# Kernel tuning notes

Measured on AMD Instinct MI355X. Metric: run time of the kernel, lower is better.

Reference implementation:

```python
import jax, jax.numpy as jnp
import numpy as np
from jax.ops import segment_sum

IN_DIM, HID_DIM, OUT_DIM = 128, 128, 64
N_NODES, N_EDGES = 50000, 800000


def gcn_conv(x, src, dst, W, b, n_nodes):
    # Symmetric GCN normalization (no self loops): deg at targets from unit weights
    deg = segment_sum(jnp.ones(src.shape[0], dtype=x.dtype), dst, num_segments=n_nodes)
    dinv = jnp.where(deg > 0, jax.lax.rsqrt(jnp.maximum(deg, 1.0)), 0.0)
    norm = dinv[src] * dinv[dst]                      # [E]
    h = x @ W                                         # [N, out] small GEMM first (PyG order)
    msg = h[src] * norm[:, None]                      # gather + scale: [E, out]
    out = segment_sum(msg, dst, num_segments=n_nodes) # scatter-add to targets
    return out + b


def setup_inputs() -> dict:
    key = jax.random.key(0)
    k1, k2, k3, k4, k5 = jax.random.split(key, 5)
    x = jax.random.normal(k1, (N_NODES, IN_DIM), dtype=jnp.float32)
    edge_index = jax.random.randint(k2, (2, N_EDGES), 0, N_NODES, dtype=jnp.int64)
    s1 = 1.0 / np.sqrt(IN_DIM)
    s2 = 1.0 / np.sqrt(HID_DIM)
    W1 = jax.random.uniform(k3, (IN_DIM, HID_DIM), jnp.float32, -s1, s1)
    b1 = jnp.zeros((HID_DIM,), jnp.float32)
    W2 = jax.random.uniform(k4, (HID_DIM, OUT_DIM), jnp.float32, -s2, s2)
    b2 = jnp.zeros((OUT_DIM,), jnp.float32)
    return {"x": x, "edge_index": edge_index, "W1": W1, "b1": b1, "W2": W2, "b2": b2}


def reference(x, edge_index, W1, b1, W2, b2):
    n_nodes = x.shape[0]
    src, dst = edge_index[0], edge_index[1]
    h = gcn_conv(x, src, dst, W1, b1, n_nodes)
    h = jax.nn.relu(h)
    # Dropout is identity in eval mode (reference is deterministic)
    out = gcn_conv(h, src, dst, W2, b2, n_nodes)
    return out
```

## Files before the change

kernel.cpp:

```cpp
#include <hip/hip_runtime.h>

#define N_NODES 50000
#define N_EDGES 800000
#define IN_DIM  128
#define HID_DIM 128
#define OUT_DIM 64

#define NPAD 50176
#define NB 7
#define KEYS (N_NODES * NB)
#define KPAD 350208
#define NB_SCAN2 (KPAD / 1024)
#define FILLB ((N_EDGES / 4 + 255) / 256)
#define DINVB (NPAD / 256)

typedef __attribute__((ext_vector_type(8))) short bf16x8;
typedef __attribute__((ext_vector_type(4))) float f32x4;

__device__ __forceinline__ unsigned short f2bf(float f) {
    unsigned u = __float_as_uint(f);
    u += 0x7fffu + ((u >> 16) & 1u);
    return (unsigned short)(u >> 16);
}
__device__ __forceinline__ float bflo(unsigned u) { return __uint_as_float(u << 16); }
__device__ __forceinline__ float bfhi(unsigned u) { return __uint_as_float(u & 0xffff0000u); }

#define ACC8(u)  do { \
    acc[0] += bflo(u.x); acc[1] += bfhi(u.x); \
    acc[2] += bflo(u.y); acc[3] += bfhi(u.y); \
    acc[4] += bflo(u.z); acc[5] += bfhi(u.z); \
    acc[6] += bflo(u.w); acc[7] += bfhi(u.w); } while (0)


__global__ void rank_hist_kernel(const int* __restrict__ src, const int* __restrict__ dst,
                                 int* __restrict__ cnt2, int* __restrict__ rank) {
    int e = (blockIdx.x * 256 + threadIdx.x) * 4;
    if (e >= N_EDGES) return;
    int4 s4 = *(const int4*)(src + e);
    int4 d4 = *(const int4*)(dst + e);
    int k0 = d4.x * NB + (s4.x >> 13);
    int k1 = d4.y * NB + (s4.y >> 13);
    int k2 = d4.z * NB + (s4.z >> 13);
    int k3 = d4.w * NB + (s4.w >> 13);
    int r0 = atomicAdd(&cnt2[k0], 1);
    int r1 = atomicAdd(&cnt2[k1], 1);
    int r2 = atomicAdd(&cnt2[k2], 1);
    int r3 = atomicAdd(&cnt2[k3], 1);
    *(int4*)(rank + e) = make_int4(r0, r1, r2, r3);
}


__global__ __launch_bounds__(1024) void reduce_kernel(const int* __restrict__ cnt2,
                                                      int* __restrict__ blockSums) {
    __shared__ int s[1024];
    int i = blockIdx.x * 1024 + threadIdx.x;
    s[threadIdx.x] = (i < KEYS) ? cnt2[i] : 0;
    __syncthreads();
    for (int off = 512; off > 0; off >>= 1) {
        if (threadIdx.x < off) s[threadIdx.x] += s[threadIdx.x + off];
        __syncthreads();
    }
    if (threadIdx.x == 0) blockSums[blockIdx.x] = s[0];
}

__global__ __launch_bounds__(1024) void scan_kernel(const int* __restrict__ cnt2,
                                                    const int* __restrict__ blockSums,
                                                    int* __restrict__ rs) {
    __shared__ int s[1024];
    __shared__ int sums[NB_SCAN2];
    __shared__ int base_s;
    if (threadIdx.x < NB_SCAN2) sums[threadIdx.x] = blockSums[threadIdx.x];
    int i = blockIdx.x * 1024 + threadIdx.x;
    int v = (i < KEYS) ? cnt2[i] : 0;
    s[threadIdx.x] = v;
    __syncthreads();
    if (threadIdx.x == 0) {
        int run = 0;
        for (int b = 0; b < (int)blockIdx.x; ++b) run += sums[b];
        base_s = run;
    }
    for (int off = 1; off < 1024; off <<= 1) {
        int t = (threadIdx.x >= off) ? s[threadIdx.x - off] : 0;
        __syncthreads();
        s[threadIdx.x] += t;
        __syncthreads();
    }
    if (i < KEYS) rs[i] = base_s + s[threadIdx.x] - v;
}


__global__ void fill_kernel(const int* __restrict__ src, const int* __restrict__ dst,
                            const int* __restrict__ rank, const int* __restrict__ rs,
                            int* __restrict__ csr_src, int* __restrict__ rs_mut,
                            float* __restrict__ dinv,
                            const float* __restrict__ W1, const float* __restrict__ W2,
                            unsigned short* __restrict__ w1t, unsigned short* __restrict__ w2t) {
    int bid = blockIdx.x;
    if (bid < FILLB) {
        int e = (bid * 256 + threadIdx.x) * 4;
        if (e >= N_EDGES) return;
        int4 s4 = *(const int4*)(src + e);
        int4 d4 = *(const int4*)(dst + e);
        int4 r4 = *(const int4*)(rank + e);
        csr_src[rs[d4.x * NB + (s4.x >> 13)] + r4.x] = s4.x;
        csr_src[rs[d4.y * NB + (s4.y >> 13)] + r4.y] = s4.y;
        csr_src[rs[d4.z * NB + (s4.z >> 13)] + r4.z] = s4.z;
        csr_src[rs[d4.w * NB + (s4.w >> 13)] + r4.w] = s4.w;
    } else if (bid < FILLB + 16) {
        int idx = (bid - FILLB) * 256 + threadIdx.x;
        int c = idx >> 5, k4 = (idx & 31) * 4;
        ushort4 o;
        o.x = f2bf(W1[(k4 + 0) * 128 + c]);
        o.y = f2bf(W1[(k4 + 1) * 128 + c]);
        o.z = f2bf(W1[(k4 + 2) * 128 + c]);
        o.w = f2bf(W1[(k4 + 3) * 128 + c]);
        *(ushort4*)(w1t + c * 128 + k4) = o;
    } else if (bid < FILLB + 24) {
        int idx = (bid - FILLB - 16) * 256 + threadIdx.x;
        if (idx >= 64 * 32) return;
        int c = idx >> 5, k4 = (idx & 31) * 4;
        ushort4 o;
        o.x = f2bf(W2[(k4 + 0) * 64 + c]);
        o.y = f2bf(W2[(k4 + 1) * 64 + c]);
        o.z = f2bf(W2[(k4 + 2) * 64 + c]);
        o.w = f2bf(W2[(k4 + 3) * 64 + c]);
        *(ushort4*)(w2t + c * 128 + k4) = o;
    } else {
        int d = (bid - FILLB - 24) * 256 + threadIdx.x;
        if (d == 0) rs_mut[KEYS] = N_EDGES;
        if (d < N_NODES) {
            int start = rs[d * NB];
            int end = (d == N_NODES - 1) ? N_EDGES : rs[d * NB + NB];
            int deg = end - start;
            dinv[d] = (deg > 0) ? rsqrtf((float)deg) : 0.0f;
        }
    }
}


__global__ __launch_bounds__(256) void gemm1_mfma(const float* __restrict__ x,
                                                  const unsigned short* __restrict__ w1t,
                                                  const float* __restrict__ dinv,
                                                  unsigned short* __restrict__ h1b) {
    int wave = threadIdx.x >> 6;
    int lane = threadIdx.x & 63;
    int n = lane & 15, quad = lane >> 4;
    int row0 = blockIdx.x * 64 + wave * 16;

    int arow = row0 + n;
    if (arow >= N_NODES) arow = N_NODES - 1;
    const float* aptr = x + (size_t)arow * 128 + quad * 8;
    const unsigned short* bbase = w1t + (size_t)n * 128 + quad * 8;

    f32x4 acc[8];
#pragma unroll
    for (int t = 0; t < 8; ++t) acc[t] = (f32x4){0.f, 0.f, 0.f, 0.f};

#pragma unroll
    for (int w4 = 0; w4 < 4; ++w4) {
        float4 f0 = *(const float4*)(aptr + w4 * 32);
        float4 f1 = *(const float4*)(aptr + w4 * 32 + 4);
        bf16x8 af;
        af[0] = (short)f2bf(f0.x); af[1] = (short)f2bf(f0.y);
        af[2] = (short)f2bf(f0.z); af[3] = (short)f2bf(f0.w);
        af[4] = (short)f2bf(f1.x); af[5] = (short)f2bf(f1.y);
        af[6] = (short)f2bf(f1.z); af[7] = (short)f2bf(f1.w);
#pragma unroll
        for (int t = 0; t < 8; ++t) {
            bf16x8 bf = *(const bf16x8*)(bbase + (size_t)t * 2048 + w4 * 32);
            acc[t] = __builtin_amdgcn_mfma_f32_16x16x32_bf16(af, bf, acc[t], 0, 0, 0);
        }
    }

#pragma unroll
    for (int r = 0; r < 4; ++r) {
        int row = row0 + quad * 4 + r;
        if (row < N_NODES) {
            float dn = dinv[row];
            unsigned short* o = h1b + (size_t)row * 128 + n;
#pragma unroll
            for (int t = 0; t < 8; ++t) o[t * 16] = f2bf(acc[t][r] * dn);
        }
    }
}


#define A1T_STRIDE 136

__global__ __launch_bounds__(256) void agg1_gemm2_fused(const int* __restrict__ csr_src,
                                                        const int* __restrict__ rs,
                                                        const float* __restrict__ dinv,
                                                        const float* __restrict__ b1,
                                                        const unsigned short* __restrict__ h1b,
                                                        const unsigned short* __restrict__ w2t,
                                                        unsigned short* __restrict__ h2b) {
    __shared__ unsigned short a1t[16 * A1T_STRIDE];

    int node0 = blockIdx.x * 16;
    int g = threadIdx.x >> 4;
    int q = threadIdx.x & 15;
    int node = node0 + g;
    int start = rs[node * NB];
    int m = rs[node * NB + NB] - start;

    float acc[8] = {};
    int j = 0;
    for (; j + 7 < m; j += 8) {
        int s0 = csr_src[start + j];
        int s1 = csr_src[start + j + 1];
        int s2 = csr_src[start + j + 2];
        int s3 = csr_src[start + j + 3];
        int s4 = csr_src[start + j + 4];
        int s5 = csr_src[start + j + 5];
        int s6 = csr_src[start + j + 6];
        int s7 = csr_src[start + j + 7];
        uint4 u0 = ((const uint4*)(h1b + (size_t)s0 * 128))[q];
        uint4 u1 = ((const uint4*)(h1b + (size_t)s1 * 128))[q];
        uint4 u2 = ((const uint4*)(h1b + (size_t)s2 * 128))[q];
        uint4 u3 = ((const uint4*)(h1b + (size_t)s3 * 128))[q];
        uint4 u4 = ((const uint4*)(h1b + (size_t)s4 * 128))[q];
        uint4 u5 = ((const uint4*)(h1b + (size_t)s5 * 128))[q];
        uint4 u6 = ((const uint4*)(h1b + (size_t)s6 * 128))[q];
        uint4 u7 = ((const uint4*)(h1b + (size_t)s7 * 128))[q];
        ACC8(u0); ACC8(u1); ACC8(u2); ACC8(u3);
        ACC8(u4); ACC8(u5); ACC8(u6); ACC8(u7);
    }
    for (; j + 3 < m; j += 4) {
        int s0 = csr_src[start + j];
        int s1 = csr_src[start + j + 1];
        int s2 = csr_src[start + j + 2];
        int s3 = csr_src[start + j + 3];
        uint4 u0 = ((const uint4*)(h1b + (size_t)s0 * 128))[q];
        uint4 u1 = ((const uint4*)(h1b + (size_t)s1 * 128))[q];
        uint4 u2 = ((const uint4*)(h1b + (size_t)s2 * 128))[q];
        uint4 u3 = ((const uint4*)(h1b + (size_t)s3 * 128))[q];
        ACC8(u0); ACC8(u1); ACC8(u2); ACC8(u3);
    }
    for (; j < m; ++j) {
        int s0 = csr_src[start + j];
        uint4 u0 = ((const uint4*)(h1b + (size_t)s0 * 128))[q];
        ACC8(u0);
    }

    {
        float dn = dinv[node];
        float4 bA = ((const float4*)b1)[2 * q];
        float4 bB = ((const float4*)b1)[2 * q + 1];
        ushort4 oA, oB;
        oA.x = f2bf(fmaxf(acc[0] * dn + bA.x, 0.f));
        oA.y = f2bf(fmaxf(acc[1] * dn + bA.y, 0.f));
        oA.z = f2bf(fmaxf(acc[2] * dn + bA.z, 0.f));
        oA.w = f2bf(fmaxf(acc[3] * dn + bA.w, 0.f));
        oB.x = f2bf(fmaxf(acc[4] * dn + bB.x, 0.f));
        oB.y = f2bf(fmaxf(acc[5] * dn + bB.y, 0.f));
        oB.z = f2bf(fmaxf(acc[6] * dn + bB.z, 0.f));
        oB.w = f2bf(fmaxf(acc[7] * dn + bB.w, 0.f));
        ushort4* o = (ushort4*)(a1t + g * A1T_STRIDE + q * 8);
        o[0] = oA;
        o[1] = oB;
    }
    __syncthreads();

    int wave = threadIdx.x >> 6;
    int lane = threadIdx.x & 63;
    int n = lane & 15, quad = lane >> 4;
    const unsigned short* bbase = w2t + (size_t)(wave * 16 + n) * 128 + quad * 8;
    const unsigned short* abase = a1t + (size_t)n * A1T_STRIDE + quad * 8;

    f32x4 c2 = (f32x4){0.f, 0.f, 0.f, 0.f};
#pragma unroll
    for (int w4 = 0; w4 < 4; ++w4) {
        bf16x8 af = *(const bf16x8*)(abase + w4 * 32);
        bf16x8 bf = *(const bf16x8*)(bbase + w4 * 32);
        c2 = __builtin_amdgcn_mfma_f32_16x16x32_bf16(af, bf, c2, 0, 0, 0);
    }

#pragma unroll
    for (int r = 0; r < 4; ++r) {
        int row = node0 + quad * 4 + r;
        float dn = dinv[row];
        h2b[(size_t)row * 64 + wave * 16 + n] = f2bf(c2[r] * dn);
    }
}


__global__ __launch_bounds__(256) void agg2_kernel(const int* __restrict__ csr_src,
                                                   const int* __restrict__ rs,
                                                   const float* __restrict__ dinv,
                                                   const float* __restrict__ b2,
                                                   const unsigned short* __restrict__ h2b,
                                                   float* __restrict__ out) {
    int node = blockIdx.x * 4 + (threadIdx.x >> 6);
    if (node >= N_NODES) return;
    int lane = threadIdx.x & 63;
    int grp = lane >> 3;
    int q   = lane & 7;
    int start = rs[node * NB];
    int m = rs[node * NB + NB] - start;

    float acc[8] = {};

    int j = grp;
    for (; j + 8 < m; j += 16) {
        int s0 = csr_src[start + j];
        int s1 = csr_src[start + j + 8];
        uint4 u0 = ((const uint4*)(h2b + (size_t)s0 * 64))[q];
        uint4 u1 = ((const uint4*)(h2b + (size_t)s1 * 64))[q];
        ACC8(u0); ACC8(u1);
    }
    if (j < m) {
        int s0 = csr_src[start + j];
        uint4 u0 = ((const uint4*)(h2b + (size_t)s0 * 64))[q];
        ACC8(u0);
    }

#pragma unroll
    for (int d = 8; d <= 32; d <<= 1) {
#pragma unroll
        for (int c = 0; c < 8; ++c) acc[c] += __shfl_xor(acc[c], d, 64);
    }

    if (lane < 8) {
        float dn = dinv[node];
        float4 bA = ((const float4*)b2)[2 * q];
        float4 bB = ((const float4*)b2)[2 * q + 1];
        float4 rA, rB;
        rA.x = acc[0] * dn + bA.x;
        rA.y = acc[1] * dn + bA.y;
        rA.z = acc[2] * dn + bA.z;
        rA.w = acc[3] * dn + bA.w;
        rB.x = acc[4] * dn + bB.x;
        rB.y = acc[5] * dn + bB.y;
        rB.z = acc[6] * dn + bB.z;
        rB.w = acc[7] * dn + bB.w;
        float4* o = (float4*)(out + (size_t)node * 64);
        o[2 * q] = rA;
        o[2 * q + 1] = rB;
    }
}


extern "C" void kernel_launch(void* const* d_in, const int* in_sizes, int n_in,
                              void* d_out, int out_size, void* d_ws, size_t ws_size,
                              hipStream_t stream) {
    const float* x  = (const float*)d_in[0];
    const int*   ei = (const int*)d_in[1];
    const float* W1 = (const float*)d_in[2];
    const float* b1 = (const float*)d_in[3];
    const float* W2 = (const float*)d_in[4];
    const float* b2 = (const float*)d_in[5];
    float* out = (float*)d_out;

    const int* src = ei;
    const int* dst = ei + N_EDGES;

    char* ws = (char*)d_ws;
    int*   cnt2      = (int*)ws;
    int*   rs        = cnt2 + KPAD;
    int*   blockSums = rs + KPAD;
    float* dinv      = (float*)(blockSums + 384);
    int*   rank      = (int*)(dinv + NPAD);
    int*   csr_src   = rank + N_EDGES;
    unsigned short* h1b = (unsigned short*)(csr_src + N_EDGES);
    unsigned short* h2b = h1b + (size_t)N_NODES * HID_DIM;
    unsigned short* w1t = h2b + (size_t)N_NODES * OUT_DIM;
    unsigned short* w2t = w1t + 128 * 128;

    hipMemsetAsync(cnt2, 0, KPAD * sizeof(int), stream);
    rank_hist_kernel<<<(N_EDGES / 4 + 255) / 256, 256, 0, stream>>>(src, dst, cnt2, rank);

    reduce_kernel<<<NB_SCAN2, 1024, 0, stream>>>(cnt2, blockSums);
    scan_kernel<<<NB_SCAN2, 1024, 0, stream>>>(cnt2, blockSums, rs);

    fill_kernel<<<FILLB + 24 + DINVB, 256, 0, stream>>>(src, dst, rank, rs, csr_src,
                                                        rs, dinv, W1, W2, w1t, w2t);

    gemm1_mfma<<<(N_NODES + 63) / 64, 256, 0, stream>>>(x, w1t, dinv, h1b);

    agg1_gemm2_fused<<<N_NODES / 16, 256, 0, stream>>>(csr_src, rs, dinv, b1, h1b, w2t, h2b);

    agg2_kernel<<<(N_NODES + 3) / 4, 256, 0, stream>>>(csr_src, rs, dinv, b2, h2b, out);
}
```

Baseline: 214.6 us.

## Compute dinv from histogram early and fuse CSR fill with GEMM1 launch

Degree normalization is now computed directly from the per-key histogram counts, inside a new prep kernel that also holds the block reduction and the weight transposes. This lets the CSR fill and the first MFMA GEMM run as one launch, since neither depends on the other, removing a kernel boundary and letting both overlap. The 8-wide unrolled gather loop in the layer-1 aggregation is also removed, leaving the 4-wide loop, which may reduce memory-level parallelism.

Result: faster. 208.8 us (-2.7%).

```diff
diff --git a/kernel.cpp b/kernel.cpp
--- a/kernel.cpp
+++ b/kernel.cpp
@@ -12,7 +12,8 @@
 #define KPAD 350208
 #define NB_SCAN2 (KPAD / 1024)
 #define FILLB ((N_EDGES / 4 + 255) / 256)
-#define DINVB (NPAD / 256)
+#define GEMM1B ((N_NODES + 63) / 64)
+#define DINVB ((N_NODES + 1023) / 1024)
 
 typedef __attribute__((ext_vector_type(8))) short bf16x8;
 typedef __attribute__((ext_vector_type(4))) float f32x4;
@@ -50,18 +51,54 @@
 }
 
 
-__global__ __launch_bounds__(1024) void reduce_kernel(const int* __restrict__ cnt2,
-                                                      int* __restrict__ blockSums) {
-    __shared__ int s[1024];
-    int i = blockIdx.x * 1024 + threadIdx.x;
-    s[threadIdx.x] = (i < KEYS) ? cnt2[i] : 0;
-    __syncthreads();
-    for (int off = 512; off > 0; off >>= 1) {
-        if (threadIdx.x < off) s[threadIdx.x] += s[threadIdx.x + off];
+__global__ __launch_bounds__(1024) void prep_kernel(const int* __restrict__ cnt2,
+                                                    int* __restrict__ blockSums,
+                                                    float* __restrict__ dinv,
+                                                    const float* __restrict__ W1,
+                                                    const float* __restrict__ W2,
+                                                    unsigned short* __restrict__ w1t,
+                                                    unsigned short* __restrict__ w2t) {
+    int bid = blockIdx.x;
+    if (bid < NB_SCAN2) {
+        __shared__ int s[1024];
+        int i = bid * 1024 + threadIdx.x;
+        s[threadIdx.x] = (i < KEYS) ? cnt2[i] : 0;
         __syncthreads();
-    }
-    if (threadIdx.x == 0) blockSums[blockIdx.x] = s[0];
-}
+        for (int off = 512; off > 0; off >>= 1) {
+            if (threadIdx.x < off) s[threadIdx.x] += s[threadIdx.x + off];
+            __syncthreads();
+        }
+        if (threadIdx.x == 0) blockSums[bid] = s[0];
+    } else if (bid < NB_SCAN2 + DINVB) {
+        int d = (bid - NB_SCAN2) * 1024 + threadIdx.x;
+        if (d < N_NODES) {
+            int base = d * NB;
+            int deg = cnt2[base] + cnt2[base + 1] + cnt2[base + 2] + cnt2[base + 3]
+                    + cnt2[base + 4] + cnt2[base + 5] + cnt2[base + 6];
+            dinv[d] = (deg > 0) ? rsqrtf((float)deg) : 0.0f;
+        }
+    } else if (bid < NB_SCAN2 + DINVB + 4) {
+        int idx = (bid - NB_SCAN2 - DINVB) * 1024 + threadIdx.x;
+        int c = idx >> 5, k4 = (idx & 31) * 4;
+        ushort4 o;
+        o.x = f2bf(W1[(k4 + 0) * 128 + c]);
+        o.y = f2bf(W1[(k4 + 1) * 128 + c]);
+        o.z = f2bf(W1[(k4 + 2) * 128 + c]);
+        o.w = f2bf(W1[(k4 + 3) * 128 + c]);
+        *(ushort4*)(w1t + c * 128 + k4) = o;
+    } else {
+        int idx = (bid - NB_SCAN2 - DINVB - 4) * 1024 + threadIdx.x;
+        if (idx >= 64 * 32) return;
+        int c = idx >> 5, k4 = (idx & 31) * 4;
+        ushort4 o;
+        o.x = f2bf(W2[(k4 + 0) * 64 + c]);
+        o.y = f2bf(W2[(k4 + 1) * 64 + c]);
+        o.z = f2bf(W2[(k4 + 2) * 64 + c]);
+        o.w = f2bf(W2[(k4 + 3) * 64 + c]);
+        *(ushort4*)(w2t + c * 128 + k4) = o;
+    }
+}
+
 
 __global__ __launch_bounds__(1024) void scan_kernel(const int* __restrict__ cnt2,
                                                     const int* __restrict__ blockSums,
@@ -70,6 +107,7 @@
     __shared__ int sums[NB_SCAN2];
     __shared__ int base_s;
     if (threadIdx.x < NB_SCAN2) sums[threadIdx.x] = blockSums[threadIdx.x];
+    if (blockIdx.x == 0 && threadIdx.x == 0) rs[KEYS] = N_EDGES;
     int i = blockIdx.x * 1024 + threadIdx.x;
     int v = (i < KEYS) ? cnt2[i] : 0;
     s[threadIdx.x] = v;
@@ -89,12 +127,15 @@
 }
 
 
-__global__ void fill_kernel(const int* __restrict__ src, const int* __restrict__ dst,
-                            const int* __restrict__ rank, const int* __restrict__ rs,
-                            int* __restrict__ csr_src, int* __restrict__ rs_mut,
-                            float* __restrict__ dinv,
-                            const float* __restrict__ W1, const float* __restrict__ W2,
-                            unsigned short* __restrict__ w1t, unsigned short* __restrict__ w2t) {
+__global__ __launch_bounds__(256) void fill_gemm1_kernel(const int* __restrict__ src,
+                                                         const int* __restrict__ dst,
+                                                         const int* __restrict__ rank,
+                                                         const int* __restrict__ rs,
+                                                         int* __restrict__ csr_src,
+                                                         const float* __restrict__ x,
+                                                         const unsigned short* __restrict__ w1t,
+                                                         const float* __restrict__ dinv,
+                                                         unsigned short* __restrict__ h1b) {
     int bid = blockIdx.x;
     if (bid < FILLB) {
         int e = (bid * 256 + threadIdx.x) * 4;
@@ -106,46 +147,14 @@
         csr_src[rs[d4.y * NB + (s4.y >> 13)] + r4.y] = s4.y;
         csr_src[rs[d4.z * NB + (s4.z >> 13)] + r4.z] = s4.z;
         csr_src[rs[d4.w * NB + (s4.w >> 13)] + r4.w] = s4.w;
-    } else if (bid < FILLB + 16) {
-        int idx = (bid - FILLB) * 256 + threadIdx.x;
-        int c = idx >> 5, k4 = (idx & 31) * 4;
-        ushort4 o;
-        o.x = f2bf(W1[(k4 + 0) * 128 + c]);
-        o.y = f2bf(W1[(k4 + 1) * 128 + c]);
-        o.z = f2bf(W1[(k4 + 2) * 128 + c]);
-        o.w = f2bf(W1[(k4 + 3) * 128 + c]);
-        *(ushort4*)(w1t + c * 128 + k4) = o;
-    } else if (bid < FILLB + 24) {
-        int idx = (bid - FILLB - 16) * 256 + threadIdx.x;
-        if (idx >= 64 * 32) return;
-        int c = idx >> 5, k4 = (idx & 31) * 4;
-        ushort4 o;
-        o.x = f2bf(W2[(k4 + 0) * 64 + c]);
-        o.y = f2bf(W2[(k4 + 1) * 64 + c]);
-        o.z = f2bf(W2[(k4 + 2) * 64 + c]);
-        o.w = f2bf(W2[(k4 + 3) * 64 + c]);
-        *(ushort4*)(w2t + c * 128 + k4) = o;
-    } else {
-        int d = (bid - FILLB - 24) * 256 + threadIdx.x;
-        if (d == 0) rs_mut[KEYS] = N_EDGES;
-        if (d < N_NODES) {
-            int start = rs[d * NB];
-            int end = (d == N_NODES - 1) ? N_EDGES : rs[d * NB + NB];
-            int deg = end - start;
-            dinv[d] = (deg > 0) ? rsqrtf((float)deg) : 0.0f;
-        }
-    }
-}
-
-
-__global__ __launch_bounds__(256) void gemm1_mfma(const float* __restrict__ x,
-                                                  const unsigned short* __restrict__ w1t,
-                                                  const float* __restrict__ dinv,
-                                                  unsigned short* __restrict__ h1b) {
+        return;
+    }
+
+    int gb = bid - FILLB;
     int wave = threadIdx.x >> 6;
     int lane = threadIdx.x & 63;
     int n = lane & 15, quad = lane >> 4;
-    int row0 = blockIdx.x * 64 + wave * 16;
+    int row0 = gb * 64 + wave * 16;
 
     int arow = row0 + n;
     if (arow >= N_NODES) arow = N_NODES - 1;
@@ -205,26 +214,6 @@
 
     float acc[8] = {};
     int j = 0;
-    for (; j + 7 < m; j += 8) {
-        int s0 = csr_src[start + j];
-        int s1 = csr_src[start + j + 1];
-        int s2 = csr_src[start + j + 2];
-        int s3 = csr_src[start + j + 3];
-        int s4 = csr_src[start + j + 4];
-        int s5 = csr_src[start + j + 5];
-        int s6 = csr_src[start + j + 6];
-        int s7 = csr_src[start + j + 7];
-        uint4 u0 = ((const uint4*)(h1b + (size_t)s0 * 128))[q];
-        uint4 u1 = ((const uint4*)(h1b + (size_t)s1 * 128))[q];
-        uint4 u2 = ((const uint4*)(h1b + (size_t)s2 * 128))[q];
-        uint4 u3 = ((const uint4*)(h1b + (size_t)s3 * 128))[q];
-        uint4 u4 = ((const uint4*)(h1b + (size_t)s4 * 128))[q];
-        uint4 u5 = ((const uint4*)(h1b + (size_t)s5 * 128))[q];
-        uint4 u6 = ((const uint4*)(h1b + (size_t)s6 * 128))[q];
-        uint4 u7 = ((const uint4*)(h1b + (size_t)s7 * 128))[q];
-        ACC8(u0); ACC8(u1); ACC8(u2); ACC8(u3);
-        ACC8(u4); ACC8(u5); ACC8(u6); ACC8(u7);
-    }
     for (; j + 3 < m; j += 4) {
         int s0 = csr_src[start + j];
         int s1 = csr_src[start + j + 1];
@@ -367,15 +356,16 @@
     unsigned short* w2t = w1t + 128 * 128;
 
     hipMemsetAsync(cnt2, 0, KPAD * sizeof(int), stream);
+
     rank_hist_kernel<<<(N_EDGES / 4 + 255) / 256, 256, 0, stream>>>(src, dst, cnt2, rank);
 
-    reduce_kernel<<<NB_SCAN2, 1024, 0, stream>>>(cnt2, blockSums);
+    prep_kernel<<<NB_SCAN2 + DINVB + 6, 1024, 0, stream>>>(cnt2, blockSums, dinv,
+                                                           W1, W2, w1t, w2t);
+
     scan_kernel<<<NB_SCAN2, 1024, 0, stream>>>(cnt2, blockSums, rs);
 
-    fill_kernel<<<FILLB + 24 + DINVB, 256, 0, stream>>>(src, dst, rank, rs, csr_src,
-                                                        rs, dinv, W1, W2, w1t, w2t);
-
-    gemm1_mfma<<<(N_NODES + 63) / 64, 256, 0, stream>>>(x, w1t, dinv, h1b);
+    fill_gemm1_kernel<<<FILLB + GEMM1B, 256, 0, stream>>>(src, dst, rank, rs, csr_src,
+                                                          x, w1t, dinv, h1b);
 
     agg1_gemm2_fused<<<N_NODES / 16, 256, 0, stream>>>(csr_src, rs, dinv, b1, h1b, w2t, h2b);
 
```
